# Kernel tuning notes

Measured on AMD Instinct MI355X. Metric: run time of the kernel, lower is better.

Reference implementation:

```python
import jax, jax.numpy as jnp
import numpy as np

B = 1_000_000
N_DIR, N_TRIAL = 2, 4
ALPHA, R_GAS, EPS = 0.3, 8.314462618, 1e-12
TAU_CLIP, LN_CLIP = 10.0, 20.0
EPS_FD, SIGMA, MARGIN = 1e-4, 0.05, 0.0
LAM_PHY, LAM_GD, LAM_TPD = 1.0, 0.1, 0.1


def renorm3(x):
    # clamp to >=0 and normalize so components sum to 1 (last axis)
    x = jnp.maximum(x, 0.0)
    return x / jnp.maximum(x.sum(-1, keepdims=True), EPS)


def nrtl_ln_gamma(x, T, g):
    # x: (B,3), T: (B,), g: (B,3,3) -> ln_gamma: (B,3)
    x = jnp.maximum(x, 0.0)
    Tc = jnp.maximum(T, 1.0)
    tau = jnp.clip(g / (R_GAS * jnp.maximum(Tc, EPS)[:, None, None]), -TAU_CLIP, TAU_CLIP)
    G = jnp.exp(-ALPHA * tau)
    denom = jnp.maximum(jnp.einsum('bj,bji->bi', x, G), EPS)          # (B,3)
    A = jnp.einsum('bj,bji->bi', x, tau * G)                          # (B,3), == num1 in torch
    term1 = A / denom
    W = x[:, None, :] * G / denom[:, None, :]                         # (B,3,3)
    inside = tau - (A / denom)[:, None, :]
    term2 = (W * inside).sum(-1)
    return jnp.clip(term1 + term2, -LN_CLIP, LN_CLIP)


def setup_inputs() -> dict:
    key = jax.random.key(0)
    k1, k2, k3, k4, k5, k6 = jax.random.split(key, 6)
    pred = jax.random.uniform(k1, (B, 6), dtype=jnp.float32, minval=0.01, maxval=1.0)
    target = jax.random.uniform(k2, (B, 6), dtype=jnp.float32, minval=0.01, maxval=1.0)
    T = 298.0 + 100.0 * jax.random.uniform(k3, (B,), dtype=jnp.float32)  # Kelvin
    g = 800.0 * jax.random.normal(k4, (B, 3, 3), dtype=jnp.float32)      # J/mol
    # simplex directions: zero-sum, unit-norm (matches _sample_simplex_directions)
    v = jax.random.normal(k5, (N_DIR, B, 3), dtype=jnp.float32)
    v = v - v.mean(-1, keepdims=True)
    dirs = v / jnp.maximum(jnp.linalg.norm(v, axis=-1, keepdims=True), 1e-12)
    noise = SIGMA * jax.random.normal(k6, (N_TRIAL, B, 3), dtype=jnp.float32)
    return {'pred': pred, 'target': target, 'T': T, 'g': g, 'dirs': dirs, 'noise': noise}


def reference(pred, target, T, g, dirs, noise):
    # supervised MSE on (E+R) compositions
    L_sup = jnp.mean((pred - target) ** 2)

    xE = renorm3(pred[:, :3])
    xR = renorm3(pred[:, 3:])
    ln_gE = nrtl_ln_gamma(xE, T, g)
    ln_gR = nrtl_ln_gamma(xR, T, g)
    # chemical potential residual r_k = ln(xE_k gE_k) - ln(xR_k gR_k)
    r = jnp.log(jnp.maximum(xE, EPS)) + ln_gE - (jnp.log(jnp.maximum(xR, EPS)) + ln_gR)
    L_phy = jnp.mean(r ** 2)

    lg = jax.vmap(lambda xx: nrtl_ln_gamma(xx, T, g))  # over trial/direction axis

    # Gibbs-Duhem finite-difference penalty along simplex directions
    x_p = renorm3(xE[None] + EPS_FD * dirs)            # (N_DIR,B,3)
    x_m = renorm3(xE[None] - EPS_FD * dirs)
    d_ln = (lg(x_p) - lg(x_m)) / (2.0 * EPS_FD)
    gd = (xE[None] * d_ln).sum(-1)                     # (N_DIR,B)
    L_gd = jnp.mean(gd * gd)

    # TPD stability penalty
    w = renorm3(xE[None] + noise)                      # (N_TRIAL,B,3)
    ln_gw = lg(w)
    tpd = (w * (jnp.log(jnp.maximum(w, EPS)) + ln_gw
                - jnp.log(jnp.maximum(xE, EPS))[None] - ln_gE[None])).sum(-1)
    L_tpd = jnp.mean(jnp.maximum(MARGIN - tpd, 0.0))

    return L_sup + LAM_PHY * L_phy + LAM_GD * L_gd + LAM_TPD * L_tpd
```

## Files before the change

### kernel.cpp

```cpp
#include <hip/hip_runtime.h>


constexpr float ALPHA    = 0.3f;
constexpr float R_GAS    = 8.314462618f;
constexpr float EPS      = 1e-12f;
constexpr float TAU_CLIP = 10.0f;
constexpr float LN_CLIP  = 20.0f;
constexpr float EPS_FD   = 1e-4f;
constexpr float LAM_PHY  = 1.0f;
constexpr float LAM_GD   = 0.1f;
constexpr float LAM_TPD  = 0.1f;

constexpr float LOG2E = 1.44269504088896340736f;
constexpr float LN2   = 0.69314718055994530942f;

__device__ __forceinline__ float clipf(float v, float lo, float hi) {
    return fminf(fmaxf(v, lo), hi);
}
__device__ __forceinline__ float fast_rcp(float x) { return __builtin_amdgcn_rcpf(x); }
__device__ __forceinline__ float fast_exp(float x) { return __expf(x); }
__device__ __forceinline__ float fast_log(float x) { return __logf(x); }

struct Mats {
    float tau[3][3];
    float G[3][3];
    float tG[3][3];
};

__device__ __forceinline__ void ln_gamma3(const float x[3], const Mats& M, float lg[3]) {
    float ratio[3], invd[3];
#pragma unroll
    for (int i = 0; i < 3; ++i) {
        float d = x[0] * M.G[0][i] + x[1] * M.G[1][i] + x[2] * M.G[2][i];
        d = fmaxf(d, EPS);
        float A = x[0] * M.tG[0][i] + x[1] * M.tG[1][i] + x[2] * M.tG[2][i];
        float inv = fast_rcp(d);
        invd[i] = inv;
        ratio[i] = A * inv;
    }
#pragma unroll
    for (int i = 0; i < 3; ++i) {
        float s = ratio[i];
#pragma unroll
        for (int j = 0; j < 3; ++j) {
            s += x[j] * M.G[i][j] * invd[j] * (M.tau[i][j] - ratio[j]);
        }
        lg[i] = clipf(s, -LN_CLIP, LN_CLIP);
    }
}

__device__ __forceinline__ void renorm3(float x[3]) {
    x[0] = fmaxf(x[0], 0.0f);
    x[1] = fmaxf(x[1], 0.0f);
    x[2] = fmaxf(x[2], 0.0f);
    float inv = fast_rcp(fmaxf(x[0] + x[1] + x[2], EPS));
    x[0] *= inv; x[1] *= inv; x[2] *= inv;
}

__global__ __launch_bounds__(256) void nrtl_loss_kernel(
    const float* __restrict__ pred,
    const float* __restrict__ target,
    const float* __restrict__ Tarr,
    const float* __restrict__ g,
    const float* __restrict__ dirs,
    const float* __restrict__ noise,
    float* __restrict__ partials, int B)
{
    const int i = blockIdx.x * blockDim.x + threadIdx.x;
    float contrib = 0.0f;

    if (i < B) {
        const float2* p2 = (const float2*)(pred   + i * 6);
        const float2* t2 = (const float2*)(target + i * 6);
        float sup = 0.0f;
        float p6[6];
#pragma unroll
        for (int k = 0; k < 3; ++k) {
            float2 pv = p2[k];
            float2 tv = t2[k];
            float dx = pv.x - tv.x, dy = pv.y - tv.y;
            sup += dx * dx + dy * dy;
            p6[2 * k]     = pv.x;
            p6[2 * k + 1] = pv.y;
        }

        float xE[3] = {p6[0], p6[1], p6[2]};
        float xR[3] = {p6[3], p6[4], p6[5]};
        renorm3(xE);
        renorm3(xR);

        const float Tc = fmaxf(Tarr[i], 1.0f);
        const float invRT = fast_rcp(R_GAS * Tc);
        Mats M;
#pragma unroll
        for (int a = 0; a < 3; ++a) {
#pragma unroll
            for (int b = 0; b < 3; ++b) {
                float ta = clipf(g[i * 9 + a * 3 + b] * invRT, -TAU_CLIP, TAU_CLIP);
                float Gv = __builtin_amdgcn_exp2f((-ALPHA * LOG2E) * ta);
                M.tau[a][b] = ta;
                M.G[a][b]   = Gv;
                M.tG[a][b]  = ta * Gv;
            }
        }

        float lgE[3], lgR[3];
        ln_gamma3(xE, M, lgE);
        ln_gamma3(xR, M, lgR);

        float logxE[3];
        float phy = 0.0f;
#pragma unroll
        for (int k = 0; k < 3; ++k) {
            logxE[k] = LN2 * __builtin_amdgcn_logf(fmaxf(xE[k], EPS));
            float logxR = LN2 * __builtin_amdgcn_logf(fmaxf(xR[k], EPS));
            float r = logxE[k] + lgE[k] - logxR - lgR[k];
            phy += r * r;
        }

        float gdsum = 0.0f;
#pragma unroll
        for (int d = 0; d < 2; ++d) {
            float dv[3];
#pragma unroll
            for (int k = 0; k < 3; ++k) dv[k] = dirs[(d * B + i) * 3 + k];
            float xp[3], xm[3];
#pragma unroll
            for (int k = 0; k < 3; ++k) {
                xp[k] = xE[k] + EPS_FD * dv[k];
                xm[k] = xE[k] - EPS_FD * dv[k];
            }
            renorm3(xp);
            renorm3(xm);
            float lgp[3], lgm[3];
            ln_gamma3(xp, M, lgp);
            ln_gamma3(xm, M, lgm);
            float gd = 0.0f;
            const float inv2e = 0.5f / EPS_FD;
#pragma unroll
            for (int k = 0; k < 3; ++k) gd += xE[k] * ((lgp[k] - lgm[k]) * inv2e);
            gdsum += gd * gd;
        }

        float tpdsum = 0.0f;
#pragma unroll
        for (int t = 0; t < 4; ++t) {
            float w[3];
#pragma unroll
            for (int k = 0; k < 3; ++k) w[k] = xE[k] + noise[(t * B + i) * 3 + k];
            renorm3(w);
            float lgw[3];
            ln_gamma3(w, M, lgw);
            float tpd = 0.0f;
#pragma unroll
            for (int k = 0; k < 3; ++k) {
                float logw = LN2 * __builtin_amdgcn_logf(fmaxf(w[k], EPS));
                tpd += w[k] * (logw + lgw[k] - logxE[k] - lgE[k]);
            }
            tpdsum += fmaxf(-tpd, 0.0f);
        }

        const float invB = 1.0f / (float)B;
        contrib = invB * (sup * (1.0f / 6.0f)
                          + LAM_PHY * phy * (1.0f / 3.0f)
                          + LAM_GD  * gdsum * 0.5f
                          + LAM_TPD * tpdsum * 0.25f);
    }

#pragma unroll
    for (int off = 32; off > 0; off >>= 1)
        contrib += __shfl_down(contrib, off, 64);

    __shared__ float ssum[4];
    const int lane = threadIdx.x & 63;
    const int wid  = threadIdx.x >> 6;
    if (lane == 0) ssum[wid] = contrib;
    __syncthreads();
    if (threadIdx.x == 0) {
        partials[blockIdx.x] = ssum[0] + ssum[1] + ssum[2] + ssum[3];
    }
}

__global__ __launch_bounds__(256) void reduce_kernel(
    const float* __restrict__ partials, int n, float* __restrict__ out)
{
    double s = 0.0;
    for (int j = threadIdx.x; j < n; j += 256) s += (double)partials[j];
#pragma unroll
    for (int off = 32; off > 0; off >>= 1)
        s += __shfl_down(s, off, 64);
    __shared__ double ds[4];
    const int lane = threadIdx.x & 63;
    const int wid  = threadIdx.x >> 6;
    if (lane == 0) ds[wid] = s;
    __syncthreads();
    if (threadIdx.x == 0) out[0] = (float)(ds[0] + ds[1] + ds[2] + ds[3]);
}

extern "C" void kernel_launch(void* const* d_in, const int* in_sizes, int n_in,
                              void* d_out, int out_size, void* d_ws, size_t ws_size,
                              hipStream_t stream) {
    const float* pred   = (const float*)d_in[0];
    const float* target = (const float*)d_in[1];
    const float* Tarr   = (const float*)d_in[2];
    const float* g      = (const float*)d_in[3];
    const float* dirs   = (const float*)d_in[4];
    const float* noise  = (const float*)d_in[5];
    const int B = in_sizes[2];

    float* partials = (float*)d_ws;
    float* out      = (float*)d_out;

    const int block = 256;
    const int grid  = (B + block - 1) / block;
    nrtl_loss_kernel<<<grid, block, 0, stream>>>(pred, target, Tarr, g, dirs, noise, partials, B);
    reduce_kernel<<<1, block, 0, stream>>>(partials, grid, out);
}
```

Before: 181.6 us.

## Stage strided per-sample inputs through LDS with coalesced float4 loads

The block's pred, target, g, dirs and noise rows are copied cooperatively into shared memory with contiguous float4 loads, and each thread then reads its own stride-3/6/9 elements from LDS. This replaces uncoalesced per-thread strided global loads. Three barriers are added and the 18 KB LDS buffer is reused across phases. The larger LDS footprint may limit occupancy, and the separate staging phases serialize loads with compute.

Measured after the change: 196.0 us. 7.9% more time.

```diff
diff --git a/kernel.cpp b/kernel.cpp
--- a/kernel.cpp
+++ b/kernel.cpp
@@ -7,9 +7,6 @@
 constexpr float TAU_CLIP = 10.0f;
 constexpr float LN_CLIP  = 20.0f;
 constexpr float EPS_FD   = 1e-4f;
-constexpr float LAM_PHY  = 1.0f;
-constexpr float LAM_GD   = 0.1f;
-constexpr float LAM_TPD  = 0.1f;
 
 constexpr float LOG2E = 1.44269504088896340736f;
 constexpr float LN2   = 0.69314718055994530942f;
@@ -18,8 +15,6 @@
     return fminf(fmaxf(v, lo), hi);
 }
 __device__ __forceinline__ float fast_rcp(float x) { return __builtin_amdgcn_rcpf(x); }
-__device__ __forceinline__ float fast_exp(float x) { return __expf(x); }
-__device__ __forceinline__ float fast_log(float x) { return __logf(x); }
 
 struct Mats {
     float tau[3][3];
@@ -66,37 +61,69 @@
     const float* __restrict__ noise,
     float* __restrict__ partials, int B)
 {
-    const int i = blockIdx.x * blockDim.x + threadIdx.x;
+    __shared__ __align__(16) float s[4608];
+
+    const int t  = threadIdx.x;
+    const int s0 = blockIdx.x * 256;
+    const int ns = min(256, B - s0);
+    const int i  = s0 + t;
+    const bool valid = (t < ns);
+
+    const float invB  = 1.0f / (float)B;
+    const float SUP_W = invB * (1.0f / 6.0f);
+    const float PHY_W = invB * (1.0f / 3.0f);
+    const float GD_W  = invB * 0.1f * 0.5f;
+    const float TPD_W = invB * 0.1f * 0.25f;
+
     float contrib = 0.0f;
 
-    if (i < B) {
-        const float2* p2 = (const float2*)(pred   + i * 6);
-        const float2* t2 = (const float2*)(target + i * 6);
-        float sup = 0.0f;
+    {
+        const int npf = ns * 6;
+        const int npf4 = npf >> 2;
+        const float4* pg = (const float4*)(pred   + (size_t)s0 * 6);
+        const float4* tg = (const float4*)(target + (size_t)s0 * 6);
+        float4* sp = (float4*)s;
+        for (int j = t; j < npf4; j += 256) {
+            float4 pv = pg[j];
+            float4 tv = tg[j];
+            float dx = pv.x - tv.x, dy = pv.y - tv.y, dz = pv.z - tv.z, dw = pv.w - tv.w;
+            contrib += SUP_W * (dx * dx + dy * dy + dz * dz + dw * dw);
+            sp[j] = pv;
+        }
+        for (int j = (npf4 << 2) + t; j < npf; j += 256) {
+            float pv = pred[(size_t)s0 * 6 + j];
+            float tv = target[(size_t)s0 * 6 + j];
+            float d = pv - tv;
+            contrib += SUP_W * d * d;
+            s[j] = pv;
+        }
+        const int ngf = ns * 9;
+        const int ngf4 = ngf >> 2;
+        const float4* gg = (const float4*)(g + (size_t)s0 * 9);
+        float4* sg = (float4*)(s + 1536);
+        for (int j = t; j < ngf4; j += 256) sg[j] = gg[j];
+        for (int j = (ngf4 << 2) + t; j < ngf; j += 256) s[1536 + j] = g[(size_t)s0 * 9 + j];
+    }
+    __syncthreads();
+
+    float xE[3], lgE[3], logxE[3];
+    Mats M;
+    if (valid) {
         float p6[6];
 #pragma unroll
-        for (int k = 0; k < 3; ++k) {
-            float2 pv = p2[k];
-            float2 tv = t2[k];
-            float dx = pv.x - tv.x, dy = pv.y - tv.y;
-            sup += dx * dx + dy * dy;
-            p6[2 * k]     = pv.x;
-            p6[2 * k + 1] = pv.y;
-        }
-
-        float xE[3] = {p6[0], p6[1], p6[2]};
+        for (int k = 0; k < 6; ++k) p6[k] = s[t * 6 + k];
         float xR[3] = {p6[3], p6[4], p6[5]};
+        xE[0] = p6[0]; xE[1] = p6[1]; xE[2] = p6[2];
         renorm3(xE);
         renorm3(xR);
 
         const float Tc = fmaxf(Tarr[i], 1.0f);
         const float invRT = fast_rcp(R_GAS * Tc);
-        Mats M;
 #pragma unroll
         for (int a = 0; a < 3; ++a) {
 #pragma unroll
             for (int b = 0; b < 3; ++b) {
-                float ta = clipf(g[i * 9 + a * 3 + b] * invRT, -TAU_CLIP, TAU_CLIP);
+                float ta = clipf(s[1536 + t * 9 + a * 3 + b] * invRT, -TAU_CLIP, TAU_CLIP);
                 float Gv = __builtin_amdgcn_exp2f((-ALPHA * LOG2E) * ta);
                 M.tau[a][b] = ta;
                 M.G[a][b]   = Gv;
@@ -104,11 +131,10 @@
             }
         }
 
-        float lgE[3], lgR[3];
+        float lgR[3];
         ln_gamma3(xE, M, lgE);
         ln_gamma3(xR, M, lgR);
 
-        float logxE[3];
         float phy = 0.0f;
 #pragma unroll
         for (int k = 0; k < 3; ++k) {
@@ -117,13 +143,39 @@
             float r = logxE[k] + lgE[k] - logxR - lgR[k];
             phy += r * r;
         }
-
+        contrib += PHY_W * phy;
+    }
+    __syncthreads();
+
+    {
+#pragma unroll
+        for (int d = 0; d < 2; ++d) {
+            const int nf = ns * 3, nf4 = nf >> 2;
+            const float* gsrc = dirs + ((size_t)d * B + s0) * 3;
+            const float4* g4 = (const float4*)gsrc;
+            float4* d4 = (float4*)(s + d * 768);
+            for (int j = t; j < nf4; j += 256) d4[j] = g4[j];
+            for (int j = (nf4 << 2) + t; j < nf; j += 256) s[d * 768 + j] = gsrc[j];
+        }
+#pragma unroll
+        for (int tr = 0; tr < 4; ++tr) {
+            const int nf = ns * 3, nf4 = nf >> 2;
+            const float* gsrc = noise + ((size_t)tr * B + s0) * 3;
+            const float4* g4 = (const float4*)gsrc;
+            float4* d4 = (float4*)(s + 1536 + tr * 768);
+            for (int j = t; j < nf4; j += 256) d4[j] = g4[j];
+            for (int j = (nf4 << 2) + t; j < nf; j += 256) s[1536 + tr * 768 + j] = gsrc[j];
+        }
+    }
+    __syncthreads();
+
+    if (valid) {
         float gdsum = 0.0f;
 #pragma unroll
         for (int d = 0; d < 2; ++d) {
             float dv[3];
 #pragma unroll
-            for (int k = 0; k < 3; ++k) dv[k] = dirs[(d * B + i) * 3 + k];
+            for (int k = 0; k < 3; ++k) dv[k] = s[d * 768 + t * 3 + k];
             float xp[3], xm[3];
 #pragma unroll
             for (int k = 0; k < 3; ++k) {
@@ -141,13 +193,14 @@
             for (int k = 0; k < 3; ++k) gd += xE[k] * ((lgp[k] - lgm[k]) * inv2e);
             gdsum += gd * gd;
         }
+        contrib += GD_W * gdsum;
 
         float tpdsum = 0.0f;
 #pragma unroll
-        for (int t = 0; t < 4; ++t) {
+        for (int tr = 0; tr < 4; ++tr) {
             float w[3];
 #pragma unroll
-            for (int k = 0; k < 3; ++k) w[k] = xE[k] + noise[(t * B + i) * 3 + k];
+            for (int k = 0; k < 3; ++k) w[k] = xE[k] + s[1536 + tr * 768 + t * 3 + k];
             renorm3(w);
             float lgw[3];
             ln_gamma3(w, M, lgw);
@@ -159,12 +212,7 @@
             }
             tpdsum += fmaxf(-tpd, 0.0f);
         }
-
-        const float invB = 1.0f / (float)B;
-        contrib = invB * (sup * (1.0f / 6.0f)
-                          + LAM_PHY * phy * (1.0f / 3.0f)
-                          + LAM_GD  * gdsum * 0.5f
-                          + LAM_TPD * tpdsum * 0.25f);
+        contrib += TPD_W * tpdsum;
     }
 
 #pragma unroll
@@ -184,15 +232,15 @@
 __global__ __launch_bounds__(256) void reduce_kernel(
     const float* __restrict__ partials, int n, float* __restrict__ out)
 {
-    double s = 0.0;
-    for (int j = threadIdx.x; j < n; j += 256) s += (double)partials[j];
+    double sacc = 0.0;
+    for (int j = threadIdx.x; j < n; j += 256) sacc += (double)partials[j];
 #pragma unroll
     for (int off = 32; off > 0; off >>= 1)
-        s += __shfl_down(s, off, 64);
+        sacc += __shfl_down(sacc, off, 64);
     __shared__ double ds[4];
     const int lane = threadIdx.x & 63;
     const int wid  = threadIdx.x >> 6;
-    if (lane == 0) ds[wid] = s;
+    if (lane == 0) ds[wid] = sacc;
     __syncthreads();
     if (threadIdx.x == 0) out[0] = (float)(ds[0] + ds[1] + ds[2] + ds[3]);
 }
```
